# Kernel optimization log

Measured on AMD Instinct MI355X. Metric: run time of the kernel, lower is better.

## Reference

```python
import jax, jax.numpy as jnp
import numpy as np

EMBED = 512
HEADS = 8
HD = EMBED // HEADS  # 64
NCLS = 1
WSIZE = 32
DIL = 2
WIN_LEN = 2 * WSIZE + 1  # 65


def setup_inputs() -> dict:
    key = jax.random.key(0)
    ks = jax.random.split(key, 5)
    B, S = 2, NCLS + 2048
    return {
        "x": jax.random.normal(ks[0], (B, S, EMBED), dtype=jnp.float32),
        "qkv_w": jax.random.normal(ks[1], (3 * EMBED, EMBED), dtype=jnp.float32) * 0.02,
        "qkv_b": jax.random.normal(ks[2], (3 * EMBED,), dtype=jnp.float32) * 0.02,
        "out_w": jax.random.normal(ks[3], (EMBED, EMBED), dtype=jnp.float32) * 0.02,
        "out_b": jax.random.normal(ks[4], (EMBED,), dtype=jnp.float32) * 0.02,
    }


def reference(x, qkv_w, qkv_b, out_w, out_b):
    B, S, E = x.shape
    P = S - NCLS  # patch_len
    scale = HD ** -0.5

    qkv = (x @ qkv_w.T + qkv_b).reshape(B, S, 3, HEADS, HD)
    qkv = qkv.transpose(2, 0, 3, 1, 4)  # (3, B, H, S, d)
    q, k, v = qkv[0], qkv[1], qkv[2]

    q_cls, k_cls, v_cls = q[:, :, :NCLS], k[:, :, :NCLS], v[:, :, :NCLS]
    q_p, k_p, v_p = q[:, :, NCLS:], k[:, :, NCLS:], v[:, :, NCLS:]

    # CLS queries: full attention over all S keys
    s_cls = jnp.einsum('bhqd,bhkd->bhqk', q_cls, k) * scale
    cls_out = jnp.einsum('bhqk,bhkd->bhqd', jax.nn.softmax(s_cls, axis=-1), v)

    # Patch queries: CLS keys + dilated local window
    pad = WSIZE * DIL
    kp = jnp.pad(k_p, ((0, 0), (0, 0), (pad, pad), (0, 0)))
    vp = jnp.pad(v_p, ((0, 0), (0, 0), (pad, pad), (0, 0)))
    idx = jnp.arange(P)[:, None] + jnp.arange(WIN_LEN)[None, :] * DIL  # (P, WL)
    kw = kp[:, :, idx]  # (B, H, P, WL, d)
    vw = vp[:, :, idx]

    sw = jnp.einsum('bhpd,bhpwd->bhpw', q_p, kw) * scale
    pos = jnp.arange(P)[:, None] + (jnp.arange(WIN_LEN) - WSIZE)[None, :] * DIL
    in_bounds = (pos >= 0) & (pos < P)  # (P, WL)
    sw = jnp.where(in_bounds[None, None], sw, -jnp.inf)
    sc = jnp.einsum('bhpd,bhcd->bhpc', q_p, k_cls) * scale

    attn = jax.nn.softmax(jnp.concatenate([sc, sw], axis=-1), axis=-1)
    a_c, a_w = attn[..., :NCLS], attn[..., NCLS:]
    patch_out = (jnp.einsum('bhpc,bhcd->bhpd', a_c, v_cls)
                 + jnp.einsum('bhpw,bhpwd->bhpd', a_w, vw))

    out = jnp.concatenate([cls_out, patch_out], axis=2)  # (B, H, S, d)
    out = out.transpose(0, 2, 1, 3).reshape(B, S, E)
    return out @ out_w.T + out_b
```

## Files before the change

kernel.cpp:

```cpp
#include <hip/hip_runtime.h>
#include <math.h>

#define S_LEN 2049
#define P_LEN 2048
#define EMB 512
#define NH 8
#define HD 64
#define SCALE 0.125f

typedef _Float16 f16x8 __attribute__((ext_vector_type(8)));
typedef float f32x4 __attribute__((ext_vector_type(4)));
typedef unsigned short u16x8 __attribute__((ext_vector_type(8)));

__device__ inline unsigned short f2h(float f) {
  _Float16 h = (_Float16)f;
  return __builtin_bit_cast(unsigned short, h);
}
__device__ inline float h2f(unsigned short u) {
  return (float)__builtin_bit_cast(_Float16, u);
}

__device__ inline float wave_sum64(float v) {
#pragma unroll
  for (int off = 32; off > 0; off >>= 1) v += __shfl_xor(v, off, 64);
  return v;
}

__device__ inline void gld16(const unsigned* g, unsigned* l) {
  __builtin_amdgcn_global_load_lds(
      (const __attribute__((address_space(1))) unsigned*)g,
      (__attribute__((address_space(3))) unsigned*)l, 16, 0, 0);
}

__global__ __launch_bounds__(256) void cvt3_f16(
    const float* __restrict__ s0, unsigned short* __restrict__ d0, int n0,
    const float* __restrict__ s1, unsigned short* __restrict__ d1, int n1,
    const float* __restrict__ s2, unsigned short* __restrict__ d2, int n2) {
  int idx = (blockIdx.x * 256 + threadIdx.x) * 8;
  const float* s;
  unsigned short* d;
  int off;
  if (idx < n0) {
    s = s0; d = d0; off = idx;
  } else if (idx < n0 + n1) {
    s = s1; d = d1; off = idx - n0;
  } else if (idx < n0 + n1 + n2) {
    s = s2; d = d2; off = idx - n0 - n1;
  } else {
    return;
  }
  float4 f0 = *(const float4*)(s + off);
  float4 f1 = *(const float4*)(s + off + 4);
  float ff[8] = {f0.x, f0.y, f0.z, f0.w, f1.x, f1.y, f1.z, f1.w};
  u16x8 vh;
#pragma unroll
  for (int e = 0; e < 8; e++) vh[e] = f2h(ff[e]);
  *(u16x8*)(d + off) = vh;
}

template <int BM, int BN, bool F16OUT>
__global__ __launch_bounds__(256) void gemm_f16(
    const unsigned short* __restrict__ A, const unsigned short* __restrict__ B,
    const float* __restrict__ bias, void* __restrict__ Cv, int M, int N,
    int KP) {
  constexpr int BK = 64;
  __shared__ __align__(16) unsigned short As[BM * BK];
  __shared__ __align__(16) unsigned short Bs[BN * BK];
  const int t = threadIdx.x;
  const int lane = t & 63, wv = t >> 6;
  const int m0 = blockIdx.x * BM, n0 = blockIdx.y * BN;
  constexpr int WM = BM / 2, WN = BN / 2;
  constexpr int RM = WM / 16, RN = WN / 16;
  const int wm = wv & 1, wn = wv >> 1;
  const int lm = lane & 15, lq = lane >> 4;

  f32x4 acc[RM][RN];
#pragma unroll
  for (int i = 0; i < RM; i++)
#pragma unroll
    for (int j = 0; j < RN; j++) acc[i][j] = (f32x4){0.f, 0.f, 0.f, 0.f};

  const int lr = lane >> 3;
  const int lc = (lane & 7) ^ lr;

  const unsigned* aptr[BM / 32];
#pragma unroll
  for (int p = 0; p < BM / 32; p++) {
    int ra = wv * (BM / 4) + p * 8 + lr;
    int gr = m0 + ra;
    gr = gr < M ? gr : M - 1;
    aptr[p] = (const unsigned*)(A + (size_t)gr * KP + lc * 8);
  }
  const unsigned* bptr[BN / 32];
#pragma unroll
  for (int p = 0; p < BN / 32; p++) {
    int rb = wv * (BN / 4) + p * 8 + lr;
    bptr[p] = (const unsigned*)(B + (size_t)(n0 + rb) * KP + lc * 8);
  }

  for (int kt = 0; kt < KP; kt += BK) {
    __syncthreads();
#pragma unroll
    for (int p = 0; p < BM / 32; p++)
      gld16(aptr[p] + (kt >> 1), (unsigned*)&As[(wv * (BM / 4) + p * 8) * BK]);
#pragma unroll
    for (int p = 0; p < BN / 32; p++)
      gld16(bptr[p] + (kt >> 1), (unsigned*)&Bs[(wv * (BN / 4) + p * 8) * BK]);
    __syncthreads();

    f16x8 fa[2][RM], fb[2][RN];
#pragma unroll
    for (int kk = 0; kk < 2; kk++) {
      int ch = ((kk * 4 + lq) ^ (lm & 7)) * 8;
#pragma unroll
      for (int mi = 0; mi < RM; mi++) {
        int ra = wm * WM + mi * 16 + lm;
        fa[kk][mi] = *(const f16x8*)&As[ra * BK + ch];
      }
#pragma unroll
      for (int ni = 0; ni < RN; ni++) {
        int rb = wn * WN + ni * 16 + lm;
        fb[kk][ni] = *(const f16x8*)&Bs[rb * BK + ch];
      }
    }
#pragma unroll
    for (int kk = 0; kk < 2; kk++)
#pragma unroll
      for (int mi = 0; mi < RM; mi++)
#pragma unroll
        for (int ni = 0; ni < RN; ni++)
          acc[mi][ni] = __builtin_amdgcn_mfma_f32_16x16x32_f16(
              fa[kk][mi], fb[kk][ni], acc[mi][ni], 0, 0, 0);
  }

#pragma unroll
  for (int ni = 0; ni < RN; ni++) {
    int n = n0 + wn * WN + ni * 16 + lm;
    float bv = bias[n];
#pragma unroll
    for (int mi = 0; mi < RM; mi++)
#pragma unroll
      for (int r = 0; r < 4; r++) {
        int m = m0 + wm * WM + mi * 16 + lq * 4 + r;
        if (m < M) {
          float val = acc[mi][ni][r] + bv;
          if constexpr (F16OUT)
            ((unsigned short*)Cv)[(size_t)m * N + n] = f2h(val);
          else
            ((float*)Cv)[(size_t)m * N + n] = val;
        }
      }
  }
}

__global__ __launch_bounds__(256) void patch_attn3(
    const unsigned short* __restrict__ qkv16,
    unsigned short* __restrict__ Aatt) {
  constexpr int LDK = 72;
  constexpr int LDT = 168;
  __shared__ __align__(16) unsigned short Ks[144 * LDK];
  __shared__ __align__(16) unsigned short Vt[64 * LDT];
  __shared__ __align__(16) unsigned short Ps[64 * LDT];

  const int t = threadIdx.x;
  const int lane = t & 63, wv = t >> 6;
  const int lm = lane & 15, lq = lane >> 4;
  const int qb = blockIdx.x;
  const int h = blockIdx.y;
  const int par = blockIdx.z & 1, b = blockIdx.z >> 1;
  const unsigned short* base = qkv16 + (size_t)b * S_LEN * 1536;
  const int qc0 = qb * 64;

  {
    uint4 z = {0, 0, 0, 0};
    for (int i = t; i < 144 * LDK / 8; i += 256) ((uint4*)Ks)[i] = z;
    for (int i = t; i < 64 * LDT / 8; i += 256) ((uint4*)Vt)[i] = z;
    for (int i = t; i < 64 * LDT / 8; i += 256) ((uint4*)Ps)[i] = z;
  }
  __syncthreads();

  {
    int rr = t >> 4;
    int cc = (t & 15) * 4;
#pragma unroll
    for (int pass = 0; pass < 8; pass++) {
      int r = pass * 16 + rr;
      int jc = qc0 - 32 + r;
      uint2 kv = {0, 0};
      if ((unsigned)jc < 1024u)
        kv = *(const uint2*)(base + (size_t)(1 + 2 * jc + par) * 1536 + 512 +
                             h * 64 + cc);
      *(uint2*)&Ks[r * LDK + cc] = kv;
    }
    if (rr == 0)
      *(uint2*)&Ks[128 * LDK + cc] =
          *(const uint2*)(base + 512 + h * 64 + cc);
  }
#pragma unroll
  for (int pass = 0; pass < 4; pass++) {
    int task = pass * 256 + t;
    int jp = task >> 4;
    int d0 = (task & 15) * 4;
    int jc0 = qc0 - 32 + 2 * jp;
    uint2 a = {0, 0}, c = {0, 0};
    if ((unsigned)jc0 < 1024u)
      a = *(const uint2*)(base + (size_t)(1 + 2 * jc0 + par) * 1536 + 1024 +
                          h * 64 + d0);
    if ((unsigned)(jc0 + 1) < 1024u)
      c = *(const uint2*)(base + (size_t)(1 + 2 * (jc0 + 1) + par) * 1536 +
                          1024 + h * 64 + d0);
    *(unsigned*)&Vt[(d0 + 0) * LDT + 2 * jp] = (a.x & 0xffffu) | (c.x << 16);
    *(unsigned*)&Vt[(d0 + 1) * LDT + 2 * jp] = (a.x >> 16) | (c.x & 0xffff0000u);
    *(unsigned*)&Vt[(d0 + 2) * LDT + 2 * jp] = (a.y & 0xffffu) | (c.y << 16);
    *(unsigned*)&Vt[(d0 + 3) * LDT + 2 * jp] = (a.y >> 16) | (c.y & 0xffff0000u);
  }
  if (t < 64) Vt[t * LDT + 128] = base[1024 + h * 64 + t];

  const int qi = wv * 16 + lm;
  const unsigned short* qg =
      base + (size_t)(1 + 2 * (qc0 + qi) + par) * 1536 + h * 64;
  f16x8 qf[2];
  qf[0] = *(const f16x8*)&qg[lq * 8];
  qf[1] = *(const f16x8*)&qg[32 + lq * 8];
  __syncthreads();

  f32x4 s[9];
#pragma unroll
  for (int nt = 0; nt < 9; nt++) s[nt] = (f32x4){0.f, 0.f, 0.f, 0.f};
#pragma unroll
  for (int nt = 0; nt < 9; nt++) {
#pragma unroll
    for (int kk = 0; kk < 2; kk++) {
      f16x8 kb = *(const f16x8*)&Ks[(nt * 16 + lm) * LDK + kk * 32 + lq * 8];
      s[nt] =
          __builtin_amdgcn_mfma_f32_16x16x32_f16(qf[kk], kb, s[nt], 0, 0, 0);
    }
  }

  float L[4];
#pragma unroll
  for (int r = 0; r < 4; r++) {
    int qrow = wv * 16 + lq * 4 + r;
    float sv[9];
    float mx = -1e30f;
#pragma unroll
    for (int nt = 0; nt < 9; nt++) {
      int jl = nt * 16 + lm;
      bool valid =
          (jl == 128) ||
          (jl < 128 && jl >= qrow && jl <= qrow + 64 &&
           (unsigned)(qc0 - 32 + jl) < 1024u);
      sv[nt] = valid ? s[nt][r] * SCALE : -1e30f;
      mx = fmaxf(mx, sv[nt]);
    }
#pragma unroll
    for (int off = 1; off < 16; off <<= 1)
      mx = fmaxf(mx, __shfl_xor(mx, off, 16));
    float l = 0.f;
#pragma unroll
    for (int nt = 0; nt < 9; nt++) {
      float e = __expf(sv[nt] - mx);
      l += e;
      Ps[qrow * LDT + nt * 16 + lm] = f2h(e);
    }
#pragma unroll
    for (int off = 1; off < 16; off <<= 1) l += __shfl_xor(l, off, 16);
    L[r] = l;
  }
  __syncthreads();

  f32x4 oa[4];
#pragma unroll
  for (int nt = 0; nt < 4; nt++) oa[nt] = (f32x4){0.f, 0.f, 0.f, 0.f};
#pragma unroll
  for (int kc = 0; kc < 5; kc++) {
    f16x8 pa = *(const f16x8*)&Ps[(wv * 16 + lm) * LDT + kc * 32 + lq * 8];
#pragma unroll
    for (int nt = 0; nt < 4; nt++) {
      f16x8 vb = *(const f16x8*)&Vt[(nt * 16 + lm) * LDT + kc * 32 + lq * 8];
      oa[nt] = __builtin_amdgcn_mfma_f32_16x16x32_f16(pa, vb, oa[nt], 0, 0, 0);
    }
  }

#pragma unroll
  for (int r = 0; r < 4; r++) {
    float inv = 1.f / L[r];
    int qrow = wv * 16 + lq * 4 + r;
    int pp = 2 * (qc0 + qrow) + par;
    unsigned short* ab = Aatt + ((size_t)b * S_LEN + 1 + pp) * 512 + h * 64;
#pragma unroll
    for (int nt = 0; nt < 4; nt++) ab[nt * 16 + lm] = f2h(oa[nt][r] * inv);
  }
}

__global__ __launch_bounds__(256) void cls_part_k(
    const unsigned short* __restrict__ qkv16, float* __restrict__ Pm,
    float* __restrict__ Pl, float* __restrict__ Po) {
  const int lane = threadIdx.x & 63;
  const int wv = threadIdx.x >> 6;
  const int ck = blockIdx.x;
  const int h = blockIdx.y;
  const int b = blockIdx.z;
  const unsigned short* base = qkv16 + (size_t)b * S_LEN * 1536;
  float qd = h2f(base[h * 64 + lane]) * SCALE;

  int c0 = ck * 64;
  int cend = (ck == 31) ? S_LEN : c0 + 64;

  float m = -1e30f, l = 0.f, o = 0.f;
  for (int j = c0 + wv; j < cend; j += 4) {
    const unsigned short* krow = base + (size_t)j * 1536 + 512 + h * 64;
    float kv = h2f(krow[lane]);
    float vv = h2f(krow[512 + lane]);
    float s = wave_sum64(qd * kv);
    float mn = fmaxf(m, s);
    float e0 = __expf(m - mn);
    float e1 = __expf(s - mn);
    l = l * e0 + e1;
    o = o * e0 + e1 * vv;
    m = mn;
  }

  __shared__ float sm[4], sl[4], so[4][64];
  if (lane == 0) {
    sm[wv] = m;
    sl[wv] = l;
  }
  so[wv][lane] = o;
  __syncthreads();
  if (wv == 0) {
    float M = -1e30f;
#pragma unroll
    for (int i = 0; i < 4; i++) M = fmaxf(M, sm[i]);
    float L = 0.f, O = 0.f;
#pragma unroll
    for (int i = 0; i < 4; i++) {
      float c = __expf(sm[i] - M);
      L += sl[i] * c;
      O += so[i][lane] * c;
    }
    int idx = (b * NH + h) * 32 + ck;
    if (lane == 0) {
      Pm[idx] = M;
      Pl[idx] = L;
    }
    Po[(size_t)idx * 64 + lane] = O;
  }
}

__global__ __launch_bounds__(64) void cls_comb_k(
    const float* __restrict__ Pm, const float* __restrict__ Pl,
    const float* __restrict__ Po, unsigned short* __restrict__ Aatt) {
  const int lane = threadIdx.x;
  const int h = blockIdx.x % NH;
  const int b = blockIdx.x / NH;
  float m = -1e30f, l = 0.f, o = 0.f;
  for (int ck = 0; ck < 32; ck++) {
    int idx = (b * NH + h) * 32 + ck;
    float mc = Pm[idx];
    float lc = Pl[idx];
    float oc = Po[(size_t)idx * 64 + lane];
    float mn = fmaxf(m, mc);
    float e0 = __expf(m - mn);
    float e1 = __expf(mc - mn);
    l = l * e0 + lc * e1;
    o = o * e0 + oc * e1;
    m = mn;
  }
  Aatt[(size_t)b * S_LEN * 512 + h * HD + lane] = f2h(o / l);
}

extern "C" void kernel_launch(void* const* d_in, const int* in_sizes, int n_in,
                              void* d_out, int out_size, void* d_ws,
                              size_t ws_size, hipStream_t stream) {
  const float* x = (const float*)d_in[0];
  const float* qkv_w = (const float*)d_in[1];
  const float* qkv_b = (const float*)d_in[2];
  const float* out_w = (const float*)d_in[3];
  const float* out_b = (const float*)d_in[4];
  float* out = (float*)d_out;

  const int M = 2 * S_LEN;

  float* cls_pm = (float*)d_ws;
  float* cls_pl = cls_pm + 512;
  float* cls_po = cls_pl + 512;
  unsigned short* Xp = (unsigned short*)(cls_po + 32768);
  unsigned short* Wq = Xp + (size_t)M * 512;
  unsigned short* Wo = Wq + (size_t)1536 * 512;
  unsigned short* Aatt = Wo + (size_t)512 * 512;
  unsigned short* qkv16 = Aatt + (size_t)M * 512;

  const int n0 = M * EMB;
  const int n1 = 1536 * EMB;
  const int n2 = EMB * EMB;
  int cvt_blocks = ((n0 + n1 + n2) / 8 + 255) / 256;
  cvt3_f16<<<cvt_blocks, 256, 0, stream>>>(x, Xp, n0, qkv_w, Wq, n1, out_w, Wo,
                                           n2);

  dim3 gq((M + 63) / 64, 1536 / 128);
  gemm_f16<64, 128, true><<<gq, 256, 0, stream>>>(Xp, Wq, qkv_b, qkv16, M,
                                                  1536, 512);

  cls_part_k<<<dim3(32, NH, 2), 256, 0, stream>>>(qkv16, cls_pm, cls_pl,
                                                  cls_po);
  cls_comb_k<<<2 * NH, 64, 0, stream>>>(cls_pm, cls_pl, cls_po, Aatt);
  patch_attn3<<<dim3(16, NH, 4), 256, 0, stream>>>(qkv16, Aatt);

  dim3 go((M + 63) / 64, EMB / 64);
  gemm_f16<64, 64, false><<<go, 256, 0, stream>>>(Aatt, Wo, out_b, out, M, EMB,
                                                  512);
}
```

Baseline: 122.0 us.

## Double-buffer GEMM shared tiles and fold CLS combine into patch attention

The f16 GEMM now uses two shared-memory buffers so the next K tile is loaded while MFMAs run on the current one, leaving one barrier per iteration instead of two. The separate cls_comb_k launch is removed, and its softmax-merge work now runs in the first block of each (batch, head) of patch_attn3. This cuts a kernel launch and hides some global-load latency, at the cost of doubled GEMM LDS use, which may lower occupancy. Whether gld16 is asynchronous decides how much overlap the GEMM actually gets.

```diff
diff --git a/kernel.cpp b/kernel.cpp
--- a/kernel.cpp
+++ b/kernel.cpp
@@ -64,8 +64,8 @@
     const float* __restrict__ bias, void* __restrict__ Cv, int M, int N,
     int KP) {
   constexpr int BK = 64;
-  __shared__ __align__(16) unsigned short As[BM * BK];
-  __shared__ __align__(16) unsigned short Bs[BN * BK];
+  __shared__ __align__(16) unsigned short As[2][BM * BK];
+  __shared__ __align__(16) unsigned short Bs[2][BN * BK];
   const int t = threadIdx.x;
   const int lane = t & 63, wv = t >> 6;
   const int m0 = blockIdx.x * BM, n0 = blockIdx.y * BN;
@@ -98,15 +98,23 @@
     bptr[p] = (const unsigned*)(B + (size_t)(n0 + rb) * KP + lc * 8);
   }
 
+  auto stage = [&](int buf, int kt) {
+#pragma unroll
+    for (int p = 0; p < BM / 32; p++)
+      gld16(aptr[p] + (kt >> 1),
+            (unsigned*)&As[buf][(wv * (BM / 4) + p * 8) * BK]);
+#pragma unroll
+    for (int p = 0; p < BN / 32; p++)
+      gld16(bptr[p] + (kt >> 1),
+            (unsigned*)&Bs[buf][(wv * (BN / 4) + p * 8) * BK]);
+  };
+
+  stage(0, 0);
+  __syncthreads();
+
+  int cur = 0;
   for (int kt = 0; kt < KP; kt += BK) {
-    __syncthreads();
-#pragma unroll
-    for (int p = 0; p < BM / 32; p++)
-      gld16(aptr[p] + (kt >> 1), (unsigned*)&As[(wv * (BM / 4) + p * 8) * BK]);
-#pragma unroll
-    for (int p = 0; p < BN / 32; p++)
-      gld16(bptr[p] + (kt >> 1), (unsigned*)&Bs[(wv * (BN / 4) + p * 8) * BK]);
-    __syncthreads();
+    if (kt + BK < KP) stage(cur ^ 1, kt + BK);
 
     f16x8 fa[2][RM], fb[2][RN];
 #pragma unroll
@@ -115,12 +123,12 @@
 #pragma unroll
       for (int mi = 0; mi < RM; mi++) {
         int ra = wm * WM + mi * 16 + lm;
-        fa[kk][mi] = *(const f16x8*)&As[ra * BK + ch];
+        fa[kk][mi] = *(const f16x8*)&As[cur][ra * BK + ch];
       }
 #pragma unroll
       for (int ni = 0; ni < RN; ni++) {
         int rb = wn * WN + ni * 16 + lm;
-        fb[kk][ni] = *(const f16x8*)&Bs[rb * BK + ch];
+        fb[kk][ni] = *(const f16x8*)&Bs[cur][rb * BK + ch];
       }
     }
 #pragma unroll
@@ -131,6 +139,9 @@
         for (int ni = 0; ni < RN; ni++)
           acc[mi][ni] = __builtin_amdgcn_mfma_f32_16x16x32_f16(
               fa[kk][mi], fb[kk][ni], acc[mi][ni], 0, 0, 0);
+
+    __syncthreads();
+    cur ^= 1;
   }
 
 #pragma unroll
@@ -154,8 +165,9 @@
 }
 
 __global__ __launch_bounds__(256) void patch_attn3(
-    const unsigned short* __restrict__ qkv16,
-    unsigned short* __restrict__ Aatt) {
+    const unsigned short* __restrict__ qkv16, unsigned short* __restrict__ Aatt,
+    const float* __restrict__ Pm, const float* __restrict__ Pl,
+    const float* __restrict__ Po) {
   constexpr int LDK = 72;
   constexpr int LDT = 168;
   __shared__ __align__(16) unsigned short Ks[144 * LDK];
@@ -291,6 +303,23 @@
 #pragma unroll
     for (int nt = 0; nt < 4; nt++) ab[nt * 16 + lm] = f2h(oa[nt][r] * inv);
   }
+
+  if (qb == 0 && par == 0 && t < 64) {
+    float m = -1e30f, l = 0.f, o = 0.f;
+    for (int ck = 0; ck < 32; ck++) {
+      int idx = (b * NH + h) * 32 + ck;
+      float mc = Pm[idx];
+      float lc = Pl[idx];
+      float oc = Po[(size_t)idx * 64 + t];
+      float mn = fmaxf(m, mc);
+      float e0 = __expf(m - mn);
+      float e1 = __expf(mc - mn);
+      l = l * e0 + lc * e1;
+      o = o * e0 + oc * e1;
+      m = mn;
+    }
+    Aatt[(size_t)b * S_LEN * 512 + h * HD + t] = f2h(o / l);
+  }
 }
 
 __global__ __launch_bounds__(256) void cls_part_k(
@@ -348,28 +377,6 @@
   }
 }
 
-__global__ __launch_bounds__(64) void cls_comb_k(
-    const float* __restrict__ Pm, const float* __restrict__ Pl,
-    const float* __restrict__ Po, unsigned short* __restrict__ Aatt) {
-  const int lane = threadIdx.x;
-  const int h = blockIdx.x % NH;
-  const int b = blockIdx.x / NH;
-  float m = -1e30f, l = 0.f, o = 0.f;
-  for (int ck = 0; ck < 32; ck++) {
-    int idx = (b * NH + h) * 32 + ck;
-    float mc = Pm[idx];
-    float lc = Pl[idx];
-    float oc = Po[(size_t)idx * 64 + lane];
-    float mn = fmaxf(m, mc);
-    float e0 = __expf(m - mn);
-    float e1 = __expf(mc - mn);
-    l = l * e0 + lc * e1;
-    o = o * e0 + oc * e1;
-    m = mn;
-  }
-  Aatt[(size_t)b * S_LEN * 512 + h * HD + lane] = f2h(o / l);
-}
-
 extern "C" void kernel_launch(void* const* d_in, const int* in_sizes, int n_in,
                               void* d_out, int out_size, void* d_ws,
                               size_t ws_size, hipStream_t stream) {
@@ -404,8 +411,8 @@
 
   cls_part_k<<<dim3(32, NH, 2), 256, 0, stream>>>(qkv16, cls_pm, cls_pl,
                                                   cls_po);
-  cls_comb_k<<<2 * NH, 64, 0, stream>>>(cls_pm, cls_pl, cls_po, Aatt);
-  patch_attn3<<<dim3(16, NH, 4), 256, 0, stream>>>(qkv16, Aatt);
+  patch_attn3<<<dim3(16, NH, 4), 256, 0, stream>>>(qkv16, Aatt, cls_pm, cls_pl,
+                                                   cls_po);
 
   dim3 go((M + 63) / 64, EMB / 64);
   gemm_f16<64, 64, false><<<go, 256, 0, stream>>>(Aatt, Wo, out_b, out, M, EMB,
```

Measured after the change: 124.2 us. Within noise of the previous version (+1.8%).
